# Kernel tuning notes

Hardware: AMD Instinct MI355X
Metric: run time of the kernel (lower is better)

Reference implementation:

```python
import jax, jax.numpy as jnp
import numpy as np

N, E, D = 50000, 500000, 128   # nodes, edges, input feature dim
H, F = 4, 32                    # num_heads, features_per_head (H*F == MLP output 128)


def _layer_norm(x, scale, bias, eps=1e-6):
    mu = jnp.mean(x, axis=-1, keepdims=True)
    var = jnp.var(x, axis=-1, keepdims=True)
    return (x - mu) * jax.lax.rsqrt(var + eps) * scale + bias


def setup_inputs() -> dict:
    key = jax.random.key(0)
    ks = jax.random.split(key, 6)
    s = lambda fan_in: 1.0 / np.sqrt(fan_in)
    return {
        "nodes": jax.random.normal(ks[0], (N, D), jnp.float32),
        "W1": jax.random.normal(ks[1], (D, 128), jnp.float32) * s(D),
        "b1": jnp.zeros((128,), jnp.float32),
        "ln1_scale": jnp.ones((128,), jnp.float32),
        "ln1_bias": jnp.zeros((128,), jnp.float32),
        "W2": jax.random.normal(ks[2], (128, H * F), jnp.float32) * s(128),
        "b2": jnp.zeros((H * F,), jnp.float32),
        "ln2_scale": jnp.ones((H * F,), jnp.float32),
        "ln2_bias": jnp.zeros((H * F,), jnp.float32),
        "senders": jax.random.randint(ks[3], (E,), 0, N, dtype=jnp.int32),
        "receivers": jax.random.randint(ks[4], (E,), 0, N, dtype=jnp.int32),
    }


def reference(nodes, W1, b1, ln1_scale, ln1_bias, W2, b2, ln2_scale, ln2_bias,
              senders, receivers):
    # attention_query MLP (MLPTorso: Dense -> LayerNorm -> relu, activate_final=True)
    h = jnp.maximum(_layer_norm(nodes @ W1 + b1, ln1_scale, ln1_bias), 0.0)
    h = jnp.maximum(_layer_norm(h @ W2 + b2, ln2_scale, ln2_bias), 0.0)
    q = h.reshape(N, H, F)                       # [N, H, F]

    # gather per-edge sender/receiver projections (same math as per-edge MLP)
    sent = q[senders]                            # [E, H, F]
    recv = q[receivers]                          # [E, H, F]

    # per-edge, per-head attention logits
    logits = jnp.einsum('ehf,ehf->eh', sent, recv) / jnp.sqrt(jnp.float32(F))

    # segment softmax over incoming edges of each receiver node (jraph semantics)
    seg_max = jax.ops.segment_max(logits, receivers, num_segments=N)
    seg_max = jnp.where(jnp.isfinite(seg_max), seg_max, 0.0)  # empty segments
    unnorm = jnp.exp(logits - seg_max[receivers])
    denom = jax.ops.segment_sum(unnorm, receivers, num_segments=N)
    weights = unnorm / denom[receivers]          # [E, H]

    # weighted messages, scatter-sum to receiver nodes
    messages = sent * weights[..., None]         # [E, H, F]
    agg = jax.ops.segment_sum(messages, receivers, num_segments=N)  # [N, H, F]

    # node update: activation then average over heads (avg_multi_head=True)
    out = jnp.maximum(agg, 0.0)
    return jnp.mean(out, axis=1)                 # [N, F]
```

## Files before the change

kernel.cpp:

```cpp
#include <hip/hip_runtime.h>

constexpr int D  = 128;
constexpr int NH = 4;
constexpr int NF = 32;

typedef __attribute__((ext_vector_type(8))) short bfrag;
typedef __attribute__((ext_vector_type(4))) float ffrag;

__device__ __forceinline__ unsigned short bf16h(float x) {
    unsigned u = __float_as_uint(x);
    u += 0x7fffu + ((u >> 16) & 1u);
    return (unsigned short)(u >> 16);
}
__device__ __forceinline__ float bf16tof(unsigned short h) {
    return __uint_as_float(((unsigned)h) << 16);
}

__global__ __launch_bounds__(256) void zero_cnt_kernel(int* __restrict__ p, int n)
{
    const int i4 = (blockIdx.x * blockDim.x + threadIdx.x) * 4;
    if (i4 + 3 < n) {
        *(int4*)&p[i4] = {0, 0, 0, 0};
    } else if (i4 < n) {
        for (int i = i4; i < n; ++i) p[i] = 0;
    }
}

__global__ __launch_bounds__(256) void wsplit_kernel(
    const float* __restrict__ W1, const float* __restrict__ W2,
    unsigned short* __restrict__ wt)
{
    const int L  = blockIdx.x >> 3;
    const int ct = blockIdx.x & 7;
    const float* W = L ? W2 : W1;
    const int ks   = threadIdx.x >> 6;
    const int lane = threadIdx.x & 63;
    const int lg = lane >> 4, lc = lane & 15;
    unsigned short* Hp = wt + ((size_t)(L * 2 + 0) * 32 + ct * 4 + ks) * 512 + lane * 8;
    unsigned short* Lp = wt + ((size_t)(L * 2 + 1) * 32 + ct * 4 + ks) * 512 + lane * 8;
    #pragma unroll
    for (int i = 0; i < 8; ++i) {
        const int k = ks * 32 + lg * 8 + i;
        const int c = ct * 16 + lc;
        const float v = W[(size_t)k * 128 + c];
        const unsigned short hh = bf16h(v);
        Hp[i] = hh;
        Lp[i] = bf16h(v - bf16tof(hh));
    }
}

__global__ __launch_bounds__(256, 4) void mlp_mfma_kernel(
    const float* __restrict__ X,
    const unsigned short* __restrict__ WF,
    const float* __restrict__ b1, const float* __restrict__ g1, const float* __restrict__ be1,
    const float* __restrict__ b2, const float* __restrict__ g2, const float* __restrict__ be2,
    unsigned short* __restrict__ Q, int N)
{
    constexpr int PW = 132;
    __shared__ unsigned HL[4 * 16 * PW];

    const int tid  = threadIdx.x;
    const int lane = tid & 63;
    const int wave = tid >> 6;
    const int lc   = lane & 15;
    const int lg   = lane >> 4;
    const int n0w  = (blockIdx.x * 4 + wave) * 16;
    if (n0w >= N) return;
    unsigned* hl = &HL[wave * 16 * PW];

    bfrag ah[4], al[4];
    ffrag acc[8];

    {
        const int rowx = (n0w + lc < N) ? (n0w + lc) : (N - 1);
        const float* xr = X + (size_t)rowx * 128 + lg * 8;
        #pragma unroll
        for (int ks = 0; ks < 4; ++ks) {
            const float4 a = *(const float4*)&xr[ks * 32];
            const float4 b = *(const float4*)&xr[ks * 32 + 4];
            const float f[8] = {a.x, a.y, a.z, a.w, b.x, b.y, b.z, b.w};
            #pragma unroll
            for (int i = 0; i < 8; ++i) {
                const unsigned short hh = bf16h(f[i]);
                ah[ks][i] = (short)hh;
                al[ks][i] = (short)bf16h(f[i] - bf16tof(hh));
            }
        }
    }

    auto gemm = [&](int hiBase, int loBase) {
        #pragma unroll
        for (int ct = 0; ct < 8; ++ct) {
            const unsigned short* bhp = WF + (size_t)(hiBase + ct * 4) * 512 + lane * 8;
            const unsigned short* blp = WF + (size_t)(loBase + ct * 4) * 512 + lane * 8;
            bfrag bh[4], bl[4];
            #pragma unroll
            for (int ks = 0; ks < 4; ++ks) {
                bh[ks] = *(const bfrag*)(bhp + ks * 512);
                bl[ks] = *(const bfrag*)(blp + ks * 512);
            }
            ffrag a = acc[ct];
            #pragma unroll
            for (int ks = 0; ks < 4; ++ks) {
                a = __builtin_amdgcn_mfma_f32_16x16x32_bf16(ah[ks], bh[ks], a, 0, 0, 0);
                a = __builtin_amdgcn_mfma_f32_16x16x32_bf16(ah[ks], bl[ks], a, 0, 0, 0);
                a = __builtin_amdgcn_mfma_f32_16x16x32_bf16(al[ks], bh[ks], a, 0, 0, 0);
            }
            acc[ct] = a;
        }
    };

    #pragma unroll
    for (int i = 0; i < 8; ++i) acc[i] = (ffrag){0.f, 0.f, 0.f, 0.f};
    gemm(0, 32);

    {
        float bb[8], gg[8], tt[8];
        #pragma unroll
        for (int ct = 0; ct < 8; ++ct) {
            const int col = ct * 16 + lc;
            bb[ct] = b1[col]; gg[ct] = g1[col]; tt[ct] = be1[col];
        }
        #pragma unroll
        for (int j = 0; j < 4; ++j) {
            float t[8], s = 0.f, ss = 0.f;
            #pragma unroll
            for (int ct = 0; ct < 8; ++ct) {
                t[ct] = acc[ct][j] + bb[ct];
                s += t[ct]; ss += t[ct] * t[ct];
            }
            #pragma unroll
            for (int off = 1; off <= 8; off <<= 1) {
                s  += __shfl_xor(s,  off, 16);
                ss += __shfl_xor(ss, off, 16);
            }
            const float mu   = s * (1.f / 128.f);
            const float var  = fmaxf(ss * (1.f / 128.f) - mu * mu, 0.f);
            const float rstd = rsqrtf(var + 1e-6f);
            const int row = lg * 4 + j;
            #pragma unroll
            for (int ct = 0; ct < 8; ++ct) {
                const float o = fmaxf((t[ct] - mu) * rstd * gg[ct] + tt[ct], 0.f);
                const unsigned short hh = bf16h(o);
                const unsigned short ll = bf16h(o - bf16tof(hh));
                hl[row * PW + ct * 16 + lc] = (unsigned)hh | ((unsigned)ll << 16);
            }
        }
    }

    asm volatile("s_waitcnt lgkmcnt(0)" ::: "memory");

    #pragma unroll
    for (int ks = 0; ks < 4; ++ks) {
        const uint4 r0 = *(const uint4*)&hl[lc * PW + ks * 32 + lg * 8];
        const uint4 r1 = *(const uint4*)&hl[lc * PW + ks * 32 + lg * 8 + 4];
        const unsigned rr[8] = {r0.x, r0.y, r0.z, r0.w, r1.x, r1.y, r1.z, r1.w};
        #pragma unroll
        for (int i = 0; i < 8; ++i) {
            ah[ks][i] = (short)(rr[i] & 0xffffu);
            al[ks][i] = (short)(rr[i] >> 16);
        }
    }

    #pragma unroll
    for (int i = 0; i < 8; ++i) acc[i] = (ffrag){0.f, 0.f, 0.f, 0.f};
    gemm(64, 96);

    {
        float bb[8], gg[8], tt[8];
        #pragma unroll
        for (int ct = 0; ct < 8; ++ct) {
            const int col = ct * 16 + lc;
            bb[ct] = b2[col]; gg[ct] = g2[col]; tt[ct] = be2[col];
        }
        #pragma unroll
        for (int j = 0; j < 4; ++j) {
            float t[8], s = 0.f, ss = 0.f;
            #pragma unroll
            for (int ct = 0; ct < 8; ++ct) {
                t[ct] = acc[ct][j] + bb[ct];
                s += t[ct]; ss += t[ct] * t[ct];
            }
            #pragma unroll
            for (int off = 1; off <= 8; off <<= 1) {
                s  += __shfl_xor(s,  off, 16);
                ss += __shfl_xor(ss, off, 16);
            }
            const float mu   = s * (1.f / 128.f);
            const float var  = fmaxf(ss * (1.f / 128.f) - mu * mu, 0.f);
            const float rstd = rsqrtf(var + 1e-6f);
            const int grow = n0w + lg * 4 + j;
            if (grow < N) {
                #pragma unroll
                for (int ct = 0; ct < 8; ++ct) {
                    const float o = fmaxf((t[ct] - mu) * rstd * gg[ct] + tt[ct], 0.f);
                    Q[(size_t)grow * 128 + ct * 16 + lc] = bf16h(o);
                }
            }
        }
    }
}

__global__ __launch_bounds__(256) void hist_kernel(
    const int* __restrict__ recv, int* __restrict__ cnt, int E)
{
    int i = blockIdx.x * blockDim.x + threadIdx.x;
    if (i < E) atomicAdd(&cnt[recv[i]], 1);
}

__global__ __launch_bounds__(256) void scan_blocks_kernel(
    const int* __restrict__ cnt, int* __restrict__ rowptr,
    int* __restrict__ bsum, int N)
{
    __shared__ int lds[256];
    const int tid = threadIdx.x;
    const int base = blockIdx.x * 1024 + tid * 4;
    int v0 = (base + 0 < N) ? cnt[base + 0] : 0;
    int v1 = (base + 1 < N) ? cnt[base + 1] : 0;
    int v2 = (base + 2 < N) ? cnt[base + 2] : 0;
    int v3 = (base + 3 < N) ? cnt[base + 3] : 0;
    const int tsum = v0 + v1 + v2 + v3;
    lds[tid] = tsum;
    __syncthreads();
    for (int off = 1; off < 256; off <<= 1) {
        int t = (tid >= off) ? lds[tid - off] : 0;
        __syncthreads();
        lds[tid] += t;
        __syncthreads();
    }
    int run = lds[tid] - tsum;
    if (base + 0 < N) rowptr[base + 0] = run;
    run += v0;
    if (base + 1 < N) rowptr[base + 1] = run;
    run += v1;
    if (base + 2 < N) rowptr[base + 2] = run;
    run += v2;
    if (base + 3 < N) rowptr[base + 3] = run;
    if (tid == 255) bsum[blockIdx.x] = lds[255];
}

__global__ __launch_bounds__(256) void scan_top_kernel(int* bsum, int nb)
{
    __shared__ int lds[256];
    const int tid = threadIdx.x;
    int v = (tid < nb) ? bsum[tid] : 0;
    lds[tid] = v;
    __syncthreads();
    for (int off = 1; off < 256; off <<= 1) {
        int t = (tid >= off) ? lds[tid - off] : 0;
        __syncthreads();
        lds[tid] += t;
        __syncthreads();
    }
    if (tid < nb) bsum[tid] = lds[tid] - v;
}

__global__ __launch_bounds__(256) void scan_add_kernel(
    int* __restrict__ rowptr, int* __restrict__ cursor,
    const int* __restrict__ bsum, int N, int E)
{
    int i = blockIdx.x * blockDim.x + threadIdx.x;
    if (i < N) {
        int v = rowptr[i] + bsum[i >> 10];
        rowptr[i] = v;
        cursor[i] = v;
    }
    if (i == 0) rowptr[N] = E;
}

__global__ __launch_bounds__(256) void fill_kernel(
    const int* __restrict__ senders, const int* __restrict__ receivers,
    int* __restrict__ cursor, int* __restrict__ ssend, int E)
{
    int e = blockIdx.x * blockDim.x + threadIdx.x;
    if (e < E) {
        int r = receivers[e];
        int pos = atomicAdd(&cursor[r], 1);
        ssend[pos] = senders[e];
    }
}

__global__ __launch_bounds__(256) void node_attn_kernel(
    const unsigned short* __restrict__ q, const int* __restrict__ rowptr,
    const int* __restrict__ ssend, float* __restrict__ out, int N)
{
    const int lane = threadIdx.x & 63;
    const int hl   = lane & 31;
    const int half = lane >> 5;
    const int wid  = (blockIdx.x * blockDim.x + threadIdx.x) >> 6;
    const int nw   = (gridDim.x * blockDim.x) >> 6;

    for (int n = wid; n < N; n += nw) {
        const uint2 braw = *(const uint2*)&q[(size_t)n * D + hl * 4];
        const float b0 = __uint_as_float(braw.x << 16);
        const float b1 = __uint_as_float(braw.x & 0xffff0000u);
        const float b2 = __uint_as_float(braw.y << 16);
        const float b3 = __uint_as_float(braw.y & 0xffff0000u);

        const int beg = rowptr[n], end = rowptr[n + 1];
        float m = -1e30f, l = 0.f;
        float c0 = 0.f, c1 = 0.f, c2 = 0.f, c3 = 0.f;

        int j = beg + half;
        uint2 raw = {0u, 0u};
        if (j < end)
            raw = *(const uint2*)&q[(size_t)ssend[j] * D + hl * 4];
        for (; j < end; j += 2) {
            const uint2 cur = raw;
            if (j + 2 < end)
                raw = *(const uint2*)&q[(size_t)ssend[j + 2] * D + hl * 4];
            const float a0 = __uint_as_float(cur.x << 16);
            const float a1 = __uint_as_float(cur.x & 0xffff0000u);
            const float a2 = __uint_as_float(cur.y << 16);
            const float a3 = __uint_as_float(cur.y & 0xffff0000u);
            float p = a0 * b0 + a1 * b1 + a2 * b2 + a3 * b3;
            p += __shfl_xor(p, 1);
            p += __shfl_xor(p, 2);
            p += __shfl_xor(p, 4);
            const float logit = p * 0.17677669529663687f;
            const float nm = fmaxf(m, logit);
            const float sc = __expf(m - nm);
            const float u  = __expf(logit - nm);
            l  = l * sc + u;
            c0 = c0 * sc + u * a0;
            c1 = c1 * sc + u * a1;
            c2 = c2 * sc + u * a2;
            c3 = c3 * sc + u * a3;
            m = nm;
        }

        const float om  = __shfl_xor(m, 32);
        const float ol  = __shfl_xor(l, 32);
        const float oc0 = __shfl_xor(c0, 32);
        const float oc1 = __shfl_xor(c1, 32);
        const float oc2 = __shfl_xor(c2, 32);
        const float oc3 = __shfl_xor(c3, 32);
        const float nm = fmaxf(m, om);
        const float s0 = __expf(m - nm), s1 = __expf(om - nm);
        const float lt = l * s0 + ol * s1;
        const float inv = (lt > 0.f) ? (1.f / lt) : 0.f;
        float r0 = fmaxf((c0 * s0 + oc0 * s1) * inv, 0.f);
        float r1 = fmaxf((c1 * s0 + oc1 * s1) * inv, 0.f);
        float r2 = fmaxf((c2 * s0 + oc2 * s1) * inv, 0.f);
        float r3 = fmaxf((c3 * s0 + oc3 * s1) * inv, 0.f);

        r0 += __shfl_xor(r0, 8);  r0 += __shfl_xor(r0, 16);
        r1 += __shfl_xor(r1, 8);  r1 += __shfl_xor(r1, 16);
        r2 += __shfl_xor(r2, 8);  r2 += __shfl_xor(r2, 16);
        r3 += __shfl_xor(r3, 8);  r3 += __shfl_xor(r3, 16);
        if (lane < 8) {
            float4 o = {0.25f * r0, 0.25f * r1, 0.25f * r2, 0.25f * r3};
            *(float4*)&out[(size_t)n * NF + lane * 4] = o;
        }
    }
}

extern "C" void kernel_launch(void* const* d_in, const int* in_sizes, int n_in,
                              void* d_out, int out_size, void* d_ws, size_t ws_size,
                              hipStream_t stream)
{
    const float* nodes = (const float*)d_in[0];
    const float* W1    = (const float*)d_in[1];
    const float* b1    = (const float*)d_in[2];
    const float* g1    = (const float*)d_in[3];
    const float* be1   = (const float*)d_in[4];
    const float* W2    = (const float*)d_in[5];
    const float* b2    = (const float*)d_in[6];
    const float* g2    = (const float*)d_in[7];
    const float* be2   = (const float*)d_in[8];
    const int* senders   = (const int*)d_in[9];
    const int* receivers = (const int*)d_in[10];

    const int N = in_sizes[0] / D;
    const int E = in_sizes[9];
    float* out = (float*)d_out;

    char* ws = (char*)d_ws;
    unsigned short* qb = (unsigned short*)ws; ws += (size_t)N * D * 2;
    unsigned short* wt = (unsigned short*)ws; ws += 4 * 128 * 128 * 2;
    int* cnt      = (int*)ws;    ws += (size_t)N * 4;
    int* rowptr   = (int*)ws;    ws += (size_t)(N + 2) * 4;
    int* cursor   = (int*)ws;    ws += (size_t)N * 4;
    int* bsum     = (int*)ws;    ws += 256 * 4;
    int* ssend    = (int*)ws;    ws += (size_t)E * 4;

    zero_cnt_kernel<<<(N / 4 + 255) / 256, 256, 0, stream>>>(cnt, N);

    wsplit_kernel<<<16, 256, 0, stream>>>(W1, W2, wt);
    const int nwaves = (N + 15) / 16;
    const int gblk = (nwaves + 3) / 4;
    mlp_mfma_kernel<<<gblk, 256, 0, stream>>>(nodes, wt, b1, g1, be1,
                                              b2, g2, be2, qb, N);

    const int nb = (N + 1023) / 1024;
    hist_kernel<<<(E + 255) / 256, 256, 0, stream>>>(receivers, cnt, E);
    scan_blocks_kernel<<<nb, 256, 0, stream>>>(cnt, rowptr, bsum, N);
    scan_top_kernel<<<1, 256, 0, stream>>>(bsum, nb);
    scan_add_kernel<<<(N + 255) / 256, 256, 0, stream>>>(rowptr, cursor, bsum, N, E);
    fill_kernel<<<(E + 255) / 256, 256, 0, stream>>>(senders, receivers, cursor, ssend, E);

    node_attn_kernel<<<(N + 3) / 4, 256, 0, stream>>>(qb, rowptr, ssend, out, N);
}
```

Before: 132.9 us.

## Fuse prep, histogram and scan kernels to cut launch count

Merges the weight split and count zeroing into one prep kernel. The receiver histogram now runs as extra blocks inside the MLP kernel, so the two overlap. The three-kernel scan is collapsed into one kernel where the last-arriving block does the top-level scan and adds offsets. The MFMA inner loop also loads B fragments per k-step instead of all up front, which lowers register pressure. Together these cut the launch count from nine to five, at the cost of an atomic done-counter and a serial final-block pass over N.

```diff
diff --git a/kernel.cpp b/kernel.cpp
--- a/kernel.cpp
+++ b/kernel.cpp
@@ -16,48 +16,55 @@
     return __uint_as_float(((unsigned)h) << 16);
 }
 
-__global__ __launch_bounds__(256) void zero_cnt_kernel(int* __restrict__ p, int n)
-{
-    const int i4 = (blockIdx.x * blockDim.x + threadIdx.x) * 4;
-    if (i4 + 3 < n) {
-        *(int4*)&p[i4] = {0, 0, 0, 0};
-    } else if (i4 < n) {
-        for (int i = i4; i < n; ++i) p[i] = 0;
-    }
-}
-
-__global__ __launch_bounds__(256) void wsplit_kernel(
+__global__ __launch_bounds__(256) void prep_kernel(
     const float* __restrict__ W1, const float* __restrict__ W2,
-    unsigned short* __restrict__ wt)
-{
-    const int L  = blockIdx.x >> 3;
-    const int ct = blockIdx.x & 7;
-    const float* W = L ? W2 : W1;
-    const int ks   = threadIdx.x >> 6;
-    const int lane = threadIdx.x & 63;
-    const int lg = lane >> 4, lc = lane & 15;
-    unsigned short* Hp = wt + ((size_t)(L * 2 + 0) * 32 + ct * 4 + ks) * 512 + lane * 8;
-    unsigned short* Lp = wt + ((size_t)(L * 2 + 1) * 32 + ct * 4 + ks) * 512 + lane * 8;
-    #pragma unroll
-    for (int i = 0; i < 8; ++i) {
-        const int k = ks * 32 + lg * 8 + i;
-        const int c = ct * 16 + lc;
-        const float v = W[(size_t)k * 128 + c];
-        const unsigned short hh = bf16h(v);
-        Hp[i] = hh;
-        Lp[i] = bf16h(v - bf16tof(hh));
-    }
-}
-
-__global__ __launch_bounds__(256, 4) void mlp_mfma_kernel(
+    unsigned short* __restrict__ wt, int* __restrict__ cnt, int nz)
+{
+    if (blockIdx.x < 16) {
+        const int L  = blockIdx.x >> 3;
+        const int ct = blockIdx.x & 7;
+        const float* W = L ? W2 : W1;
+        const int ks   = threadIdx.x >> 6;
+        const int lane = threadIdx.x & 63;
+        const int lg = lane >> 4, lc = lane & 15;
+        unsigned short* Hp = wt + ((size_t)(L * 2 + 0) * 32 + ct * 4 + ks) * 512 + lane * 8;
+        unsigned short* Lp = wt + ((size_t)(L * 2 + 1) * 32 + ct * 4 + ks) * 512 + lane * 8;
+        #pragma unroll
+        for (int i = 0; i < 8; ++i) {
+            const int k = ks * 32 + lg * 8 + i;
+            const int c = ct * 16 + lc;
+            const float v = W[(size_t)k * 128 + c];
+            const unsigned short hh = bf16h(v);
+            Hp[i] = hh;
+            Lp[i] = bf16h(v - bf16tof(hh));
+        }
+    } else {
+        const int i4 = ((blockIdx.x - 16) * 256 + threadIdx.x) * 4;
+        if (i4 + 3 < nz) {
+            *(int4*)&cnt[i4] = {0, 0, 0, 0};
+        } else if (i4 < nz) {
+            for (int i = i4; i < nz; ++i) cnt[i] = 0;
+        }
+    }
+}
+
+__global__ __launch_bounds__(256, 4) void mlp_hist_kernel(
     const float* __restrict__ X,
     const unsigned short* __restrict__ WF,
     const float* __restrict__ b1, const float* __restrict__ g1, const float* __restrict__ be1,
     const float* __restrict__ b2, const float* __restrict__ g2, const float* __restrict__ be2,
-    unsigned short* __restrict__ Q, int N)
+    unsigned short* __restrict__ Q, int N,
+    const int* __restrict__ recv, int* __restrict__ cnt, int E, int mlpBlocks)
 {
     constexpr int PW = 132;
     __shared__ unsigned HL[4 * 16 * PW];
+
+    if (blockIdx.x >= mlpBlocks) {
+        const int tid0   = (blockIdx.x - mlpBlocks) * 256 + threadIdx.x;
+        const int stride = (gridDim.x - mlpBlocks) * 256;
+        for (int i = tid0; i < E; i += stride) atomicAdd(&cnt[recv[i]], 1);
+        return;
+    }
 
     const int tid  = threadIdx.x;
     const int lane = tid & 63;
@@ -93,18 +100,14 @@
         for (int ct = 0; ct < 8; ++ct) {
             const unsigned short* bhp = WF + (size_t)(hiBase + ct * 4) * 512 + lane * 8;
             const unsigned short* blp = WF + (size_t)(loBase + ct * 4) * 512 + lane * 8;
-            bfrag bh[4], bl[4];
+            ffrag a = acc[ct];
             #pragma unroll
             for (int ks = 0; ks < 4; ++ks) {
-                bh[ks] = *(const bfrag*)(bhp + ks * 512);
-                bl[ks] = *(const bfrag*)(blp + ks * 512);
-            }
-            ffrag a = acc[ct];
-            #pragma unroll
-            for (int ks = 0; ks < 4; ++ks) {
-                a = __builtin_amdgcn_mfma_f32_16x16x32_bf16(ah[ks], bh[ks], a, 0, 0, 0);
-                a = __builtin_amdgcn_mfma_f32_16x16x32_bf16(ah[ks], bl[ks], a, 0, 0, 0);
-                a = __builtin_amdgcn_mfma_f32_16x16x32_bf16(al[ks], bh[ks], a, 0, 0, 0);
+                const bfrag bh = *(const bfrag*)(bhp + ks * 512);
+                const bfrag bl = *(const bfrag*)(blp + ks * 512);
+                a = __builtin_amdgcn_mfma_f32_16x16x32_bf16(ah[ks], bh, a, 0, 0, 0);
+                a = __builtin_amdgcn_mfma_f32_16x16x32_bf16(ah[ks], bl, a, 0, 0, 0);
+                a = __builtin_amdgcn_mfma_f32_16x16x32_bf16(al[ks], bh, a, 0, 0, 0);
             }
             acc[ct] = a;
         }
@@ -201,19 +204,16 @@
     }
 }
 
-__global__ __launch_bounds__(256) void hist_kernel(
-    const int* __restrict__ recv, int* __restrict__ cnt, int E)
-{
-    int i = blockIdx.x * blockDim.x + threadIdx.x;
-    if (i < E) atomicAdd(&cnt[recv[i]], 1);
-}
-
-__global__ __launch_bounds__(256) void scan_blocks_kernel(
+__global__ __launch_bounds__(256) void scan_fused_kernel(
     const int* __restrict__ cnt, int* __restrict__ rowptr,
-    int* __restrict__ bsum, int N)
+    int* __restrict__ cursor, int* __restrict__ bsum,
+    int* __restrict__ done, int N, int E)
 {
     __shared__ int lds[256];
+    __shared__ int base_s[64];
+    __shared__ int amlast;
     const int tid = threadIdx.x;
+    const int nb  = gridDim.x;
     const int base = blockIdx.x * 1024 + tid * 4;
     int v0 = (base + 0 < N) ? cnt[base + 0] : 0;
     int v1 = (base + 1 < N) ? cnt[base + 1] : 0;
@@ -237,35 +237,39 @@
     run += v2;
     if (base + 3 < N) rowptr[base + 3] = run;
     if (tid == 255) bsum[blockIdx.x] = lds[255];
-}
-
-__global__ __launch_bounds__(256) void scan_top_kernel(int* bsum, int nb)
-{
-    __shared__ int lds[256];
-    const int tid = threadIdx.x;
-    int v = (tid < nb) ? bsum[tid] : 0;
-    lds[tid] = v;
+
+    __threadfence();
     __syncthreads();
-    for (int off = 1; off < 256; off <<= 1) {
-        int t = (tid >= off) ? lds[tid - off] : 0;
-        __syncthreads();
-        lds[tid] += t;
-        __syncthreads();
-    }
-    if (tid < nb) bsum[tid] = lds[tid] - v;
-}
-
-__global__ __launch_bounds__(256) void scan_add_kernel(
-    int* __restrict__ rowptr, int* __restrict__ cursor,
-    const int* __restrict__ bsum, int N, int E)
-{
-    int i = blockIdx.x * blockDim.x + threadIdx.x;
-    if (i < N) {
-        int v = rowptr[i] + bsum[i >> 10];
+    if (tid == 0) amlast = (atomicAdd(done, 1) == nb - 1);
+    __syncthreads();
+    if (!amlast) return;
+    __threadfence();
+
+    if (tid < 64) {
+        const int own = (tid < nb) ? bsum[tid] : 0;
+        int incl = own;
+        #pragma unroll
+        for (int off = 1; off < 64; off <<= 1) {
+            const int t = __shfl_up(incl, off, 64);
+            if (tid >= off) incl += t;
+        }
+        base_s[tid] = incl - own;
+    }
+    __syncthreads();
+
+    for (int i = tid * 4; i + 3 < N; i += 1024) {
+        const int b4 = base_s[i >> 10];
+        int4 r = *(int4*)&rowptr[i];
+        r.x += b4; r.y += b4; r.z += b4; r.w += b4;
+        *(int4*)&rowptr[i] = r;
+        *(int4*)&cursor[i] = r;
+    }
+    for (int i = (N & ~3) + tid; i < N; i += 256) {
+        const int v = rowptr[i] + base_s[i >> 10];
         rowptr[i] = v;
         cursor[i] = v;
     }
-    if (i == 0) rowptr[N] = E;
+    if (tid == 0) rowptr[N] = E;
 }
 
 __global__ __launch_bounds__(256) void fill_kernel(
@@ -378,25 +382,26 @@
     char* ws = (char*)d_ws;
     unsigned short* qb = (unsigned short*)ws; ws += (size_t)N * D * 2;
     unsigned short* wt = (unsigned short*)ws; ws += 4 * 128 * 128 * 2;
-    int* cnt      = (int*)ws;    ws += (size_t)N * 4;
+    int* cnt      = (int*)ws;    ws += (size_t)(N + 16) * 4;
     int* rowptr   = (int*)ws;    ws += (size_t)(N + 2) * 4;
     int* cursor   = (int*)ws;    ws += (size_t)N * 4;
     int* bsum     = (int*)ws;    ws += 256 * 4;
     int* ssend    = (int*)ws;    ws += (size_t)E * 4;
-
-    zero_cnt_kernel<<<(N / 4 + 255) / 256, 256, 0, stream>>>(cnt, N);
-
-    wsplit_kernel<<<16, 256, 0, stream>>>(W1, W2, wt);
-    const int nwaves = (N + 15) / 16;
-    const int gblk = (nwaves + 3) / 4;
-    mlp_mfma_kernel<<<gblk, 256, 0, stream>>>(nodes, wt, b1, g1, be1,
-                                              b2, g2, be2, qb, N);
-
+    int* done     = cnt + N;
+
+    const int nz = N + 16;
+    const int zb = (nz + 1023) / 1024;
+    const int mlpBlocks = ((N + 15) / 16 + 3) / 4;
     const int nb = (N + 1023) / 1024;
-    hist_kernel<<<(E + 255) / 256, 256, 0, stream>>>(receivers, cnt, E);
-    scan_blocks_kernel<<<nb, 256, 0, stream>>>(cnt, rowptr, bsum, N);
-    scan_top_kernel<<<1, 256, 0, stream>>>(bsum, nb);
-    scan_add_kernel<<<(N + 255) / 256, 256, 0, stream>>>(rowptr, cursor, bsum, N, E);
+
+    prep_kernel<<<16 + zb, 256, 0, stream>>>(W1, W2, wt, cnt, nz);
+
+    mlp_hist_kernel<<<mlpBlocks + 128, 256, 0, stream>>>(
+        nodes, wt, b1, g1, be1, b2, g2, be2, qb, N,
+        receivers, cnt, E, mlpBlocks);
+
+    scan_fused_kernel<<<nb, 256, 0, stream>>>(cnt, rowptr, cursor, bsum, done, N, E);
+
     fill_kernel<<<(E + 255) / 256, 256, 0, stream>>>(senders, receivers, cursor, ssend, E);
 
     node_attn_kernel<<<(N + 3) / 4, 256, 0, stream>>>(qb, rowptr, ssend, out, N);
```

Result: slower. 149.7 us (+12.7%).

## Split MLP tile columns across wave pairs with shared LayerNorm reduction

Applied to the files above, without the earlier changes.

Each 16-row node tile is now handled by two waves, each computing half of the 128 output columns. LayerNorm row sums are combined through shared memory with block barriers. The MFMA chain is also split into two independent accumulators (hi and cross terms) to shorten dependency chains. This doubles the grid size and adds __syncthreads barriers and redundant input-fragment conversion per wave, in exchange for more parallelism and fewer registers per wave.

```diff
diff --git a/kernel.cpp b/kernel.cpp
--- a/kernel.cpp
+++ b/kernel.cpp
@@ -49,7 +49,7 @@
     }
 }
 
-__global__ __launch_bounds__(256, 4) void mlp_mfma_kernel(
+__global__ __launch_bounds__(256, 4) void mlp_pair_kernel(
     const float* __restrict__ X,
     const unsigned short* __restrict__ WF,
     const float* __restrict__ b1, const float* __restrict__ g1, const float* __restrict__ be1,
@@ -57,20 +57,31 @@
     unsigned short* __restrict__ Q, int N)
 {
     constexpr int PW = 132;
-    __shared__ unsigned HL[4 * 16 * PW];
+    __shared__ unsigned Scr[2][16 * PW];
+    __shared__ float Sums[2][2][16][2];
 
     const int tid  = threadIdx.x;
     const int lane = tid & 63;
     const int wave = tid >> 6;
+    const int pair = wave >> 1;
+    const int w    = wave & 1;
     const int lc   = lane & 15;
     const int lg   = lane >> 4;
-    const int n0w  = (blockIdx.x * 4 + wave) * 16;
-    if (n0w >= N) return;
-    unsigned* hl = &HL[wave * 16 * PW];
+
+    const int nwt = (N + 15) >> 4;
+    const int tileIdx = blockIdx.x * 2 + pair;
+    const bool valid = tileIdx < nwt;
+    const int n0w = (valid ? tileIdx : (nwt - 1)) * 16;
+
+    float b1v[4], g1v[4], t1v[4], b2v[4], g2v[4], t2v[4];
+    #pragma unroll
+    for (int ct = 0; ct < 4; ++ct) {
+        const int col = (w * 4 + ct) * 16 + lc;
+        b1v[ct] = b1[col]; g1v[ct] = g1[col]; t1v[ct] = be1[col];
+        b2v[ct] = b2[col]; g2v[ct] = g2[col]; t2v[ct] = be2[col];
+    }
 
     bfrag ah[4], al[4];
-    ffrag acc[8];
-
     {
         const int rowx = (n0w + lc < N) ? (n0w + lc) : (N - 1);
         const float* xr = X + (size_t)rowx * 128 + lg * 8;
@@ -88,72 +99,71 @@
         }
     }
 
-    auto gemm = [&](int hiBase, int loBase) {
-        #pragma unroll
-        for (int ct = 0; ct < 8; ++ct) {
-            const unsigned short* bhp = WF + (size_t)(hiBase + ct * 4) * 512 + lane * 8;
-            const unsigned short* blp = WF + (size_t)(loBase + ct * 4) * 512 + lane * 8;
-            bfrag bh[4], bl[4];
-            #pragma unroll
-            for (int ks = 0; ks < 4; ++ks) {
-                bh[ks] = *(const bfrag*)(bhp + ks * 512);
-                bl[ks] = *(const bfrag*)(blp + ks * 512);
-            }
-            ffrag a = acc[ct];
-            #pragma unroll
-            for (int ks = 0; ks < 4; ++ks) {
-                a = __builtin_amdgcn_mfma_f32_16x16x32_bf16(ah[ks], bh[ks], a, 0, 0, 0);
-                a = __builtin_amdgcn_mfma_f32_16x16x32_bf16(ah[ks], bl[ks], a, 0, 0, 0);
-                a = __builtin_amdgcn_mfma_f32_16x16x32_bf16(al[ks], bh[ks], a, 0, 0, 0);
-            }
-            acc[ct] = a;
-        }
-    };
-
-    #pragma unroll
-    for (int i = 0; i < 8; ++i) acc[i] = (ffrag){0.f, 0.f, 0.f, 0.f};
-    gemm(0, 32);
-
-    {
-        float bb[8], gg[8], tt[8];
-        #pragma unroll
-        for (int ct = 0; ct < 8; ++ct) {
-            const int col = ct * 16 + lc;
-            bb[ct] = b1[col]; gg[ct] = g1[col]; tt[ct] = be1[col];
-        }
-        #pragma unroll
-        for (int j = 0; j < 4; ++j) {
-            float t[8], s = 0.f, ss = 0.f;
-            #pragma unroll
-            for (int ct = 0; ct < 8; ++ct) {
-                t[ct] = acc[ct][j] + bb[ct];
-                s += t[ct]; ss += t[ct] * t[ct];
-            }
-            #pragma unroll
-            for (int off = 1; off <= 8; off <<= 1) {
-                s  += __shfl_xor(s,  off, 16);
-                ss += __shfl_xor(ss, off, 16);
-            }
-            const float mu   = s * (1.f / 128.f);
-            const float var  = fmaxf(ss * (1.f / 128.f) - mu * mu, 0.f);
-            const float rstd = rsqrtf(var + 1e-6f);
-            const int row = lg * 4 + j;
-            #pragma unroll
-            for (int ct = 0; ct < 8; ++ct) {
-                const float o = fmaxf((t[ct] - mu) * rstd * gg[ct] + tt[ct], 0.f);
-                const unsigned short hh = bf16h(o);
-                const unsigned short ll = bf16h(o - bf16tof(hh));
-                hl[row * PW + ct * 16 + lc] = (unsigned)hh | ((unsigned)ll << 16);
-            }
-        }
-    }
-
-    asm volatile("s_waitcnt lgkmcnt(0)" ::: "memory");
+    ffrag accH[4], accX[4];
+
+    #pragma unroll
+    for (int ct = 0; ct < 4; ++ct) {
+        const int ctg = w * 4 + ct;
+        const unsigned short* bhp = WF + (size_t)(0  + ctg * 4) * 512 + lane * 8;
+        const unsigned short* blp = WF + (size_t)(32 + ctg * 4) * 512 + lane * 8;
+        ffrag aH = (ffrag){0.f, 0.f, 0.f, 0.f};
+        ffrag aX = (ffrag){0.f, 0.f, 0.f, 0.f};
+        #pragma unroll
+        for (int ks = 0; ks < 4; ++ks) {
+            const bfrag bh = *(const bfrag*)(bhp + ks * 512);
+            const bfrag bl = *(const bfrag*)(blp + ks * 512);
+            aH = __builtin_amdgcn_mfma_f32_16x16x32_bf16(ah[ks], bh, aH, 0, 0, 0);
+            aX = __builtin_amdgcn_mfma_f32_16x16x32_bf16(ah[ks], bl, aX, 0, 0, 0);
+            aX = __builtin_amdgcn_mfma_f32_16x16x32_bf16(al[ks], bh, aX, 0, 0, 0);
+        }
+        accH[ct] = aH; accX[ct] = aX;
+    }
+
+    float tv[4][4];
+    #pragma unroll
+    for (int j = 0; j < 4; ++j) {
+        float s = 0.f, ss = 0.f;
+        #pragma unroll
+        for (int ct = 0; ct < 4; ++ct) {
+            const float t = accH[ct][j] + accX[ct][j] + b1v[ct];
+            tv[j][ct] = t;
+            s += t; ss += t * t;
+        }
+        #pragma unroll
+        for (int off = 1; off <= 8; off <<= 1) {
+            s  += __shfl_xor(s,  off, 16);
+            ss += __shfl_xor(ss, off, 16);
+        }
+        if (lc == 0) {
+            Sums[pair][w][lg * 4 + j][0] = s;
+            Sums[pair][w][lg * 4 + j][1] = ss;
+        }
+    }
+    __syncthreads();
+
+    #pragma unroll
+    for (int j = 0; j < 4; ++j) {
+        const int row = lg * 4 + j;
+        const float s  = Sums[pair][0][row][0] + Sums[pair][1][row][0];
+        const float ss = Sums[pair][0][row][1] + Sums[pair][1][row][1];
+        const float mu   = s * (1.f / 128.f);
+        const float var  = fmaxf(ss * (1.f / 128.f) - mu * mu, 0.f);
+        const float rstd = rsqrtf(var + 1e-6f);
+        #pragma unroll
+        for (int ct = 0; ct < 4; ++ct) {
+            const float o = fmaxf((tv[j][ct] - mu) * rstd * g1v[ct] + t1v[ct], 0.f);
+            const unsigned short hh = bf16h(o);
+            const unsigned short ll = bf16h(o - bf16tof(hh));
+            Scr[pair][row * PW + (w * 4 + ct) * 16 + lc] =
+                (unsigned)hh | ((unsigned)ll << 16);
+        }
+    }
+    __syncthreads();
 
     #pragma unroll
     for (int ks = 0; ks < 4; ++ks) {
-        const uint4 r0 = *(const uint4*)&hl[lc * PW + ks * 32 + lg * 8];
-        const uint4 r1 = *(const uint4*)&hl[lc * PW + ks * 32 + lg * 8 + 4];
+        const uint4 r0 = *(const uint4*)&Scr[pair][lc * PW + ks * 32 + lg * 8];
+        const uint4 r1 = *(const uint4*)&Scr[pair][lc * PW + ks * 32 + lg * 8 + 4];
         const unsigned rr[8] = {r0.x, r0.y, r0.z, r0.w, r1.x, r1.y, r1.z, r1.w};
         #pragma unroll
         for (int i = 0; i < 8; ++i) {
@@ -163,39 +173,58 @@
     }
 
     #pragma unroll
-    for (int i = 0; i < 8; ++i) acc[i] = (ffrag){0.f, 0.f, 0.f, 0.f};
-    gemm(64, 96);
-
-    {
-        float bb[8], gg[8], tt[8];
-        #pragma unroll
-        for (int ct = 0; ct < 8; ++ct) {
-            const int col = ct * 16 + lc;
-            bb[ct] = b2[col]; gg[ct] = g2[col]; tt[ct] = be2[col];
-        }
-        #pragma unroll
-        for (int j = 0; j < 4; ++j) {
-            float t[8], s = 0.f, ss = 0.f;
+    for (int ct = 0; ct < 4; ++ct) {
+        const int ctg = w * 4 + ct;
+        const unsigned short* bhp = WF + (size_t)(64 + ctg * 4) * 512 + lane * 8;
+        const unsigned short* blp = WF + (size_t)(96 + ctg * 4) * 512 + lane * 8;
+        ffrag aH = (ffrag){0.f, 0.f, 0.f, 0.f};
+        ffrag aX = (ffrag){0.f, 0.f, 0.f, 0.f};
+        #pragma unroll
+        for (int ks = 0; ks < 4; ++ks) {
+            const bfrag bh = *(const bfrag*)(bhp + ks * 512);
+            const bfrag bl = *(const bfrag*)(blp + ks * 512);
+            aH = __builtin_amdgcn_mfma_f32_16x16x32_bf16(ah[ks], bh, aH, 0, 0, 0);
+            aX = __builtin_amdgcn_mfma_f32_16x16x32_bf16(ah[ks], bl, aX, 0, 0, 0);
+            aX = __builtin_amdgcn_mfma_f32_16x16x32_bf16(al[ks], bh, aX, 0, 0, 0);
+        }
+        accH[ct] = aH; accX[ct] = aX;
+    }
+
+    #pragma unroll
+    for (int j = 0; j < 4; ++j) {
+        float s = 0.f, ss = 0.f;
+        #pragma unroll
+        for (int ct = 0; ct < 4; ++ct) {
+            const float t = accH[ct][j] + accX[ct][j] + b2v[ct];
+            tv[j][ct] = t;
+            s += t; ss += t * t;
+        }
+        #pragma unroll
+        for (int off = 1; off <= 8; off <<= 1) {
+            s  += __shfl_xor(s,  off, 16);
+            ss += __shfl_xor(ss, off, 16);
+        }
+        if (lc == 0) {
+            Sums[pair][w][lg * 4 + j][0] = s;
+            Sums[pair][w][lg * 4 + j][1] = ss;
+        }
+    }
+    __syncthreads();
+
+    #pragma unroll
+    for (int j = 0; j < 4; ++j) {
+        const int row = lg * 4 + j;
+        const float s  = Sums[pair][0][row][0] + Sums[pair][1][row][0];
+        const float ss = Sums[pair][0][row][1] + Sums[pair][1][row][1];
+        const float mu   = s * (1.f / 128.f);
+        const float var  = fmaxf(ss * (1.f / 128.f) - mu * mu, 0.f);
+        const float rstd = rsqrtf(var + 1e-6f);
+        const int grow = n0w + row;
+        if (valid && grow < N) {
             #pragma unroll
-            for (int ct = 0; ct < 8; ++ct) {
-                t[ct] = acc[ct][j] + bb[ct];
-                s += t[ct]; ss += t[ct] * t[ct];
-            }
-            #pragma unroll
-            for (int off = 1; off <= 8; off <<= 1) {
-                s  += __shfl_xor(s,  off, 16);
-                ss += __shfl_xor(ss, off, 16);
-            }
-            const float mu   = s * (1.f / 128.f);
-            const float var  = fmaxf(ss * (1.f / 128.f) - mu * mu, 0.f);
-            const float rstd = rsqrtf(var + 1e-6f);
-            const int grow = n0w + lg * 4 + j;
-            if (grow < N) {
-                #pragma unroll
-                for (int ct = 0; ct < 8; ++ct) {
-                    const float o = fmaxf((t[ct] - mu) * rstd * gg[ct] + tt[ct], 0.f);
-                    Q[(size_t)grow * 128 + ct * 16 + lc] = bf16h(o);
-                }
+            for (int ct = 0; ct < 4; ++ct) {
+                const float o = fmaxf((tv[j][ct] - mu) * rstd * g2v[ct] + t2v[ct], 0.f);
+                Q[(size_t)grow * 128 + (w * 4 + ct) * 16 + lc] = bf16h(o);
             }
         }
     }
@@ -387,10 +416,9 @@
     zero_cnt_kernel<<<(N / 4 + 255) / 256, 256, 0, stream>>>(cnt, N);
 
     wsplit_kernel<<<16, 256, 0, stream>>>(W1, W2, wt);
-    const int nwaves = (N + 15) / 16;
-    const int gblk = (nwaves + 3) / 4;
-    mlp_mfma_kernel<<<gblk, 256, 0, stream>>>(nodes, wt, b1, g1, be1,
-                                              b2, g2, be2, qb, N);
+    const int nwt = (N + 15) / 16;
+    mlp_pair_kernel<<<(nwt + 1) / 2, 256, 0, stream>>>(
+        nodes, wt, b1, g1, be1, b2, g2, be2, qb, N);
 
     const int nb = (N + 1023) / 1024;
     hist_kernel<<<(E + 255) / 256, 256, 0, stream>>>(receivers, cnt, E);
```

Result: slower. 136.6 us (+2.8%).

## Fuse weight prep with count zeroing, fold histogram into MLP, stage weights in LDS

Applied to the files above, without the earlier changes.

Merges the weight-split and count-zeroing kernels into one launch, and folds the receiver histogram into the MLP kernel as extra blocks so the atomics run alongside the GEMM. The MLP now stages each layer's split bf16 weights into shared memory with global_load_lds and reads the MFMA B operands from LDS rather than from global memory. It also splits the hi and cross accumulators to shorten the MFMA dependency chain. The 64KB LDS buffer lowers occupancy (launch bounds now 2) and adds block-wide barriers.

```diff
diff --git a/kernel.cpp b/kernel.cpp
--- a/kernel.cpp
+++ b/kernel.cpp
@@ -16,63 +16,76 @@
     return __uint_as_float(((unsigned)h) << 16);
 }
 
-__global__ __launch_bounds__(256) void zero_cnt_kernel(int* __restrict__ p, int n)
-{
-    const int i4 = (blockIdx.x * blockDim.x + threadIdx.x) * 4;
-    if (i4 + 3 < n) {
-        *(int4*)&p[i4] = {0, 0, 0, 0};
-    } else if (i4 < n) {
-        for (int i = i4; i < n; ++i) p[i] = 0;
-    }
-}
-
-__global__ __launch_bounds__(256) void wsplit_kernel(
+__device__ __forceinline__ void gload_lds16(const unsigned short* g, unsigned short* l)
+{
+    __builtin_amdgcn_global_load_lds(
+        (const __attribute__((address_space(1))) void*)g,
+        (__attribute__((address_space(3))) void*)l, 16, 0, 0);
+}
+
+__global__ __launch_bounds__(256) void prep_kernel(
     const float* __restrict__ W1, const float* __restrict__ W2,
-    unsigned short* __restrict__ wt)
-{
-    const int L  = blockIdx.x >> 3;
-    const int ct = blockIdx.x & 7;
-    const float* W = L ? W2 : W1;
-    const int ks   = threadIdx.x >> 6;
-    const int lane = threadIdx.x & 63;
-    const int lg = lane >> 4, lc = lane & 15;
-    unsigned short* Hp = wt + ((size_t)(L * 2 + 0) * 32 + ct * 4 + ks) * 512 + lane * 8;
-    unsigned short* Lp = wt + ((size_t)(L * 2 + 1) * 32 + ct * 4 + ks) * 512 + lane * 8;
-    #pragma unroll
-    for (int i = 0; i < 8; ++i) {
-        const int k = ks * 32 + lg * 8 + i;
-        const int c = ct * 16 + lc;
-        const float v = W[(size_t)k * 128 + c];
-        const unsigned short hh = bf16h(v);
-        Hp[i] = hh;
-        Lp[i] = bf16h(v - bf16tof(hh));
-    }
-}
-
-__global__ __launch_bounds__(256, 4) void mlp_mfma_kernel(
+    unsigned short* __restrict__ wt, int* __restrict__ cnt, int nz)
+{
+    if (blockIdx.x < 16) {
+        const int L  = blockIdx.x >> 3;
+        const int ct = blockIdx.x & 7;
+        const float* W = L ? W2 : W1;
+        const int ks   = threadIdx.x >> 6;
+        const int lane = threadIdx.x & 63;
+        const int lg = lane >> 4, lc = lane & 15;
+        unsigned short* Hp = wt + ((size_t)(L * 2 + 0) * 32 + ct * 4 + ks) * 512 + lane * 8;
+        unsigned short* Lp = wt + ((size_t)(L * 2 + 1) * 32 + ct * 4 + ks) * 512 + lane * 8;
+        #pragma unroll
+        for (int i = 0; i < 8; ++i) {
+            const int k = ks * 32 + lg * 8 + i;
+            const int c = ct * 16 + lc;
+            const float v = W[(size_t)k * 128 + c];
+            const unsigned short hh = bf16h(v);
+            Hp[i] = hh;
+            Lp[i] = bf16h(v - bf16tof(hh));
+        }
+    } else {
+        const int i4 = ((blockIdx.x - 16) * 256 + threadIdx.x) * 4;
+        if (i4 + 3 < nz) {
+            *(int4*)&cnt[i4] = {0, 0, 0, 0};
+        } else if (i4 < nz) {
+            for (int i = i4; i < nz; ++i) cnt[i] = 0;
+        }
+    }
+}
+
+__global__ __launch_bounds__(256, 2) void mlp_hist_kernel(
     const float* __restrict__ X,
     const unsigned short* __restrict__ WF,
     const float* __restrict__ b1, const float* __restrict__ g1, const float* __restrict__ be1,
     const float* __restrict__ b2, const float* __restrict__ g2, const float* __restrict__ be2,
-    unsigned short* __restrict__ Q, int N)
-{
+    unsigned short* __restrict__ Q, int N,
+    const int* __restrict__ recv, int* __restrict__ cnt, int E, int mlpBlocks)
+{
+    __shared__ unsigned short Wlds[32768];
+
+    if (blockIdx.x >= mlpBlocks) {
+        const int tid0   = (blockIdx.x - mlpBlocks) * 256 + threadIdx.x;
+        const int stride = (gridDim.x - mlpBlocks) * 256;
+        for (int i = tid0; i < E; i += stride) atomicAdd(&cnt[recv[i]], 1);
+        return;
+    }
+
     constexpr int PW = 132;
-    __shared__ unsigned HL[4 * 16 * PW];
-
     const int tid  = threadIdx.x;
     const int lane = tid & 63;
     const int wave = tid >> 6;
     const int lc   = lane & 15;
     const int lg   = lane >> 4;
-    const int n0w  = (blockIdx.x * 4 + wave) * 16;
-    if (n0w >= N) return;
-    unsigned* hl = &HL[wave * 16 * PW];
+    const int n0w  = blockIdx.x * 64 + wave * 16;
 
     bfrag ah[4], al[4];
     ffrag acc[8];
 
     {
-        const int rowx = (n0w + lc < N) ? (n0w + lc) : (N - 1);
+        const int row = n0w + lc;
+        const int rowx = (row < N) ? row : (N - 1);
         const float* xr = X + (size_t)rowx * 128 + lg * 8;
         #pragma unroll
         for (int ks = 0; ks < 4; ++ks) {
@@ -88,72 +101,81 @@
         }
     }
 
-    auto gemm = [&](int hiBase, int loBase) {
+    float b1v[8], g1v[8], t1v[8], b2v[8], g2v[8], t2v[8];
+    #pragma unroll
+    for (int ct = 0; ct < 8; ++ct) {
+        const int col = ct * 16 + lc;
+        b1v[ct] = b1[col]; g1v[ct] = g1[col]; t1v[ct] = be1[col];
+        b2v[ct] = b2[col]; g2v[ct] = g2[col]; t2v[ct] = be2[col];
+    }
+
+#define STAGE_LAYER(Lbase)                                                     \
+    {                                                                          \
+        _Pragma("unroll")                                                      \
+        for (int i_ = 0; i_ < 16; ++i_) {                                      \
+            const int ch_ = wave * 16 + i_;                                    \
+            gload_lds16(WF + ((size_t)(Lbase) + ch_) * 512 + lane * 8,         \
+                        &Wlds[ch_ * 512]);                                     \
+        }                                                                      \
+    }
+
+#define GEMM_LDS()                                                             \
+    _Pragma("unroll")                                                          \
+    for (int ct_ = 0; ct_ < 8; ++ct_) {                                        \
+        const unsigned short* bh_ = &Wlds[(ct_ * 4) * 512 + lane * 8];         \
+        const unsigned short* bl_ = &Wlds[(32 + ct_ * 4) * 512 + lane * 8];    \
+        ffrag aH_ = (ffrag){0.f,0.f,0.f,0.f}, aX_ = (ffrag){0.f,0.f,0.f,0.f};  \
+        _Pragma("unroll")                                                      \
+        for (int ks_ = 0; ks_ < 4; ++ks_) {                                    \
+            const bfrag bh = *(const bfrag*)(bh_ + ks_ * 512);                 \
+            const bfrag bl = *(const bfrag*)(bl_ + ks_ * 512);                 \
+            aH_ = __builtin_amdgcn_mfma_f32_16x16x32_bf16(ah[ks_], bh, aH_, 0, 0, 0); \
+            aX_ = __builtin_amdgcn_mfma_f32_16x16x32_bf16(ah[ks_], bl, aX_, 0, 0, 0); \
+            aX_ = __builtin_amdgcn_mfma_f32_16x16x32_bf16(al[ks_], bh, aX_, 0, 0, 0); \
+        }                                                                      \
+        acc[ct_] = aH_ + aX_;                                                  \
+    }
+
+    STAGE_LAYER(0)
+    __syncthreads();
+
+    GEMM_LDS()
+    __syncthreads();
+
+    unsigned* scr = (unsigned*)Wlds + wave * (16 * PW);
+    #pragma unroll
+    for (int j = 0; j < 4; ++j) {
+        float t[8], s = 0.f, ss = 0.f;
         #pragma unroll
         for (int ct = 0; ct < 8; ++ct) {
-            const unsigned short* bhp = WF + (size_t)(hiBase + ct * 4) * 512 + lane * 8;
-            const unsigned short* blp = WF + (size_t)(loBase + ct * 4) * 512 + lane * 8;
-            bfrag bh[4], bl[4];
-            #pragma unroll
-            for (int ks = 0; ks < 4; ++ks) {
-                bh[ks] = *(const bfrag*)(bhp + ks * 512);
-                bl[ks] = *(const bfrag*)(blp + ks * 512);
-            }
-            ffrag a = acc[ct];
-            #pragma unroll
-            for (int ks = 0; ks < 4; ++ks) {
-                a = __builtin_amdgcn_mfma_f32_16x16x32_bf16(ah[ks], bh[ks], a, 0, 0, 0);
-                a = __builtin_amdgcn_mfma_f32_16x16x32_bf16(ah[ks], bl[ks], a, 0, 0, 0);
-                a = __builtin_amdgcn_mfma_f32_16x16x32_bf16(al[ks], bh[ks], a, 0, 0, 0);
-            }
-            acc[ct] = a;
-        }
-    };
-
-    #pragma unroll
-    for (int i = 0; i < 8; ++i) acc[i] = (ffrag){0.f, 0.f, 0.f, 0.f};
-    gemm(0, 32);
-
-    {
-        float bb[8], gg[8], tt[8];
+            t[ct] = acc[ct][j] + b1v[ct];
+            s += t[ct]; ss += t[ct] * t[ct];
+        }
+        #pragma unroll
+        for (int off = 1; off <= 8; off <<= 1) {
+            s  += __shfl_xor(s,  off, 16);
+            ss += __shfl_xor(ss, off, 16);
+        }
+        const float mu   = s * (1.f / 128.f);
+        const float var  = fmaxf(ss * (1.f / 128.f) - mu * mu, 0.f);
+        const float rstd = rsqrtf(var + 1e-6f);
+        const int row = lg * 4 + j;
         #pragma unroll
         for (int ct = 0; ct < 8; ++ct) {
-            const int col = ct * 16 + lc;
-            bb[ct] = b1[col]; gg[ct] = g1[col]; tt[ct] = be1[col];
-        }
-        #pragma unroll
-        for (int j = 0; j < 4; ++j) {
-            float t[8], s = 0.f, ss = 0.f;
-            #pragma unroll
-            for (int ct = 0; ct < 8; ++ct) {
-                t[ct] = acc[ct][j] + bb[ct];
-                s += t[ct]; ss += t[ct] * t[ct];
-            }
-            #pragma unroll
-            for (int off = 1; off <= 8; off <<= 1) {
-                s  += __shfl_xor(s,  off, 16);
-                ss += __shfl_xor(ss, off, 16);
-            }
-            const float mu   = s * (1.f / 128.f);
-            const float var  = fmaxf(ss * (1.f / 128.f) - mu * mu, 0.f);
-            const float rstd = rsqrtf(var + 1e-6f);
-            const int row = lg * 4 + j;
-            #pragma unroll
-            for (int ct = 0; ct < 8; ++ct) {
-                const float o = fmaxf((t[ct] - mu) * rstd * gg[ct] + tt[ct], 0.f);
-                const unsigned short hh = bf16h(o);
-                const unsigned short ll = bf16h(o - bf16tof(hh));
-                hl[row * PW + ct * 16 + lc] = (unsigned)hh | ((unsigned)ll << 16);
-            }
+            const float o = fmaxf((t[ct] - mu) * rstd * g1v[ct] + t1v[ct], 0.f);
+            const unsigned short hh = bf16h(o);
+            const unsigned short ll = bf16h(o - bf16tof(hh));
+            scr[row * PW + ct * 16 + lc] = (unsigned)hh | ((unsigned)ll << 16);
         }
     }
 
     asm volatile("s_waitcnt lgkmcnt(0)" ::: "memory");
+    __builtin_amdgcn_sched_barrier(0);
 
     #pragma unroll
     for (int ks = 0; ks < 4; ++ks) {
-        const uint4 r0 = *(const uint4*)&hl[lc * PW + ks * 32 + lg * 8];
-        const uint4 r1 = *(const uint4*)&hl[lc * PW + ks * 32 + lg * 8 + 4];
+        const uint4 r0 = *(const uint4*)&scr[lc * PW + ks * 32 + lg * 8];
+        const uint4 r1 = *(const uint4*)&scr[lc * PW + ks * 32 + lg * 8 + 4];
         const unsigned rr[8] = {r0.x, r0.y, r0.z, r0.w, r1.x, r1.y, r1.z, r1.w};
         #pragma unroll
         for (int i = 0; i < 8; ++i) {
@@ -161,51 +183,41 @@
             al[ks][i] = (short)(rr[i] >> 16);
         }
     }
+    __syncthreads();
+
+    STAGE_LAYER(64)
+    __syncthreads();
+
+    GEMM_LDS()
+
+#undef GEMM_LDS
+#undef STAGE_LAYER
 
     #pragma unroll
-    for (int i = 0; i < 8; ++i) acc[i] = (ffrag){0.f, 0.f, 0.f, 0.f};
-    gemm(64, 96);
-
-    {
-        float bb[8], gg[8], tt[8];
+    for (int j = 0; j < 4; ++j) {
+        float t[8], s = 0.f, ss = 0.f;
         #pragma unroll
         for (int ct = 0; ct < 8; ++ct) {
-            const int col = ct * 16 + lc;
-            bb[ct] = b2[col]; gg[ct] = g2[col]; tt[ct] = be2[col];
-        }
-        #pragma unroll
-        for (int j = 0; j < 4; ++j) {
-            float t[8], s = 0.f, ss = 0.f;
+            t[ct] = acc[ct][j] + b2v[ct];
+            s += t[ct]; ss += t[ct] * t[ct];
+        }
+        #pragma unroll
+        for (int off = 1; off <= 8; off <<= 1) {
+            s  += __shfl_xor(s,  off, 16);
+            ss += __shfl_xor(ss, off, 16);
+        }
+        const float mu   = s * (1.f / 128.f);
+        const float var  = fmaxf(ss * (1.f / 128.f) - mu * mu, 0.f);
+        const float rstd = rsqrtf(var + 1e-6f);
+        const int grow = n0w + lg * 4 + j;
+        if (grow < N) {
             #pragma unroll
             for (int ct = 0; ct < 8; ++ct) {
-                t[ct] = acc[ct][j] + bb[ct];
-                s += t[ct]; ss += t[ct] * t[ct];
+                const float o = fmaxf((t[ct] - mu) * rstd * g2v[ct] + t2v[ct], 0.f);
+                Q[(size_t)grow * 128 + ct * 16 + lc] = bf16h(o);
             }
-            #pragma unroll
-            for (int off = 1; off <= 8; off <<= 1) {
-                s  += __shfl_xor(s,  off, 16);
-                ss += __shfl_xor(ss, off, 16);
-            }
-            const float mu   = s * (1.f / 128.f);
-            const float var  = fmaxf(ss * (1.f / 128.f) - mu * mu, 0.f);
-            const float rstd = rsqrtf(var + 1e-6f);
-            const int grow = n0w + lg * 4 + j;
-            if (grow < N) {
-                #pragma unroll
-                for (int ct = 0; ct < 8; ++ct) {
-                    const float o = fmaxf((t[ct] - mu) * rstd * gg[ct] + tt[ct], 0.f);
-                    Q[(size_t)grow * 128 + ct * 16 + lc] = bf16h(o);
-                }
-            }
-        }
-    }
-}
-
-__global__ __launch_bounds__(256) void hist_kernel(
-    const int* __restrict__ recv, int* __restrict__ cnt, int E)
-{
-    int i = blockIdx.x * blockDim.x + threadIdx.x;
-    if (i < E) atomicAdd(&cnt[recv[i]], 1);
+        }
+    }
 }
 
 __global__ __launch_bounds__(256) void scan_blocks_kernel(
@@ -384,19 +396,20 @@
     int* bsum     = (int*)ws;    ws += 256 * 4;
     int* ssend    = (int*)ws;    ws += (size_t)E * 4;
 
-    zero_cnt_kernel<<<(N / 4 + 255) / 256, 256, 0, stream>>>(cnt, N);
-
-    wsplit_kernel<<<16, 256, 0, stream>>>(W1, W2, wt);
-    const int nwaves = (N + 15) / 16;
-    const int gblk = (nwaves + 3) / 4;
-    mlp_mfma_kernel<<<gblk, 256, 0, stream>>>(nodes, wt, b1, g1, be1,
-                                              b2, g2, be2, qb, N);
-
+    const int zb = (N + 1023) / 1024;
+    const int mlpBlocks = (N + 63) / 64;
     const int nb = (N + 1023) / 1024;
-    hist_kernel<<<(E + 255) / 256, 256, 0, stream>>>(receivers, cnt, E);
+
+    prep_kernel<<<16 + zb, 256, 0, stream>>>(W1, W2, wt, cnt, N);
+
+    mlp_hist_kernel<<<mlpBlocks + 128, 256, 0, stream>>>(
+        nodes, wt, b1, g1, be1, b2, g2, be2, qb, N,
+        receivers, cnt, E, mlpBlocks);
+
     scan_blocks_kernel<<<nb, 256, 0, stream>>>(cnt, rowptr, bsum, N);
     scan_top_kernel<<<1, 256, 0, stream>>>(bsum, nb);
     scan_add_kernel<<<(N + 255) / 256, 256, 0, stream>>>(rowptr, cursor, bsum, N, E);
+
     fill_kernel<<<(E + 255) / 256, 256, 0, stream>>>(senders, receivers, cursor, ssend, E);
 
     node_attn_kernel<<<(N + 3) / 4, 256, 0, stream>>>(qb, rowptr, ssend, out, N);
```

Result: faster. 119.1 us (-10.3%).
